# Kernel optimization log

Hardware: AMD Instinct MI355X
Metric: run time of the kernel (lower is better)

Reference implementation:

```python
import jax, jax.numpy as jnp
import numpy as np

N_NODES = 100000
N_EDGES = 3200000
NFEAT, H1, H2, NCLASS = 512, 300, 200, 40


def setup_inputs() -> dict:
    key = jax.random.key(0)
    ks = jax.random.split(key, 8)
    x = jax.random.normal(ks[0], (N_NODES, NFEAT), dtype=jnp.float32)
    edge_index = jax.random.randint(ks[1], (2, N_EDGES), 0, N_NODES, dtype=jnp.int32)
    edge_weight = jax.random.uniform(ks[2], (N_EDGES,), dtype=jnp.float32)
    def glorot(k, fi, fo):
        s = 1.0 / np.sqrt(fi)
        return jax.random.uniform(k, (fi, fo), jnp.float32, -s, s)
    w1 = glorot(ks[3], NFEAT, H1)
    w2 = glorot(ks[4], H1, H2)
    w3 = glorot(ks[5], H2, NCLASS)
    return {
        'x': x, 'edge_index': edge_index, 'edge_weight': edge_weight,
        'w1': w1, 'b1': jnp.zeros((H1,), jnp.float32),
        'w2': w2, 'b2': jnp.zeros((H2,), jnp.float32),
        'w3': w3, 'b3': jnp.zeros((NCLASS,), jnp.float32),
    }


def _gcn_layer(h, edge_index, edge_weight, w, b):
    # support = h @ W ; out = A @ support + b  (A given as weighted edge list)
    support = h @ w                                   # [N, out]
    src, dst = edge_index[0], edge_index[1]
    msgs = support[src] * edge_weight[:, None]        # gather + scale, [E, out]
    agg = jax.ops.segment_sum(msgs, dst, num_segments=h.shape[0])
    return agg + b


def reference(x, edge_index, edge_weight, w1, b1, w2, b2, w3, b3):
    h1 = jax.nn.relu(_gcn_layer(x, edge_index, edge_weight, w1, b1))
    h2 = jax.nn.relu(_gcn_layer(h1, edge_index, edge_weight, w2, b2))
    logits = _gcn_layer(h2, edge_index, edge_weight, w3, b3)
    return jax.nn.softmax(logits, axis=1)
```

## Files before the change

kernel.cpp:

```cpp
#include <hip/hip_runtime.h>
#include <hip/hip_bf16.h>
#include <hip/hip_fp16.h>
#include <math.h>

#define NFEAT 512
#define H1 300
#define H2 200
#define NCLASS 40

typedef __attribute__((ext_vector_type(8))) _Float16 half8;
typedef __attribute__((ext_vector_type(4))) float f32x4;
typedef __attribute__((ext_vector_type(2))) unsigned int u32x2;

__device__ __forceinline__ void stage16(const void* gptr, void* ldsptr) {
    __builtin_amdgcn_global_load_lds(
        (const __attribute__((address_space(1))) unsigned int*)gptr,
        (__attribute__((address_space(3))) unsigned int*)ldsptr,
        16, 0, 0);
}

__device__ __forceinline__ unsigned short f2h(float f) {
    return __half_as_ushort(__float2half(f));
}
__device__ __forceinline__ float h2f(unsigned short u) {
    return __half2float(__ushort_as_half(u));
}
__device__ __forceinline__ float2 h2f2(unsigned int u) {
    __half2 h = *reinterpret_cast<__half2*>(&u);
    return __half22float2(h);
}
__device__ __forceinline__ unsigned pack2h(float a, float b) {
    return (unsigned)f2h(a) | ((unsigned)f2h(b) << 16);
}


__global__ __launch_bounds__(256) void count_dst_kernel(const int* __restrict__ dst,
                                                        int* __restrict__ counts, int E) {
    int i = blockIdx.x * blockDim.x + threadIdx.x;
    if (i < E) atomicAdd(&counts[dst[i]], 1);
}

__global__ __launch_bounds__(1024) void scan_kernel(const int* __restrict__ counts,
                                                    int* __restrict__ row_ptr,
                                                    int* __restrict__ nextp, int N) {
    __shared__ int sums[1024];
    const int tid = threadIdx.x;
    const int CH = (N + 1023) >> 10;
    const int b = tid * CH;
    const int e = min(b + CH, N);
    int s = 0;
    for (int i = b; i < e; i++) s += counts[i];
    sums[tid] = s;
    __syncthreads();
    #pragma unroll
    for (int off = 1; off < 1024; off <<= 1) {
        int t = (tid >= off) ? sums[tid - off] : 0;
        __syncthreads();
        sums[tid] += t;
        __syncthreads();
    }
    int run = (tid > 0) ? sums[tid - 1] : 0;
    for (int i = b; i < e; i++) {
        row_ptr[i] = run;
        nextp[i] = run;
        run += counts[i];
    }
    if (tid == 0) row_ptr[N] = sums[1023];
}


__global__ __launch_bounds__(256) void fill_csr_pass_kernel(const int* __restrict__ src,
                                                            const int* __restrict__ dst,
                                                            const float* __restrict__ ew,
                                                            int* __restrict__ next,
                                                            int2* __restrict__ csr_sw,
                                                            int E, int lo, int hi) {
    int i = blockIdx.x * blockDim.x + threadIdx.x;
    if (i < E) {
        int d = dst[i];
        if (d >= lo && d < hi) {
            int pos = atomicAdd(&next[d], 1);
            csr_sw[pos] = make_int2(src[i], __float_as_int(ew[i]));
        }
    }
}


__global__ __launch_bounds__(256) void split_weights_kernel(
        const float* __restrict__ w1, const float* __restrict__ w2, const float* __restrict__ w3,
        unsigned short* __restrict__ W1H, unsigned short* __restrict__ W1L,
        unsigned short* __restrict__ W2H, unsigned short* __restrict__ W2L,
        unsigned short* __restrict__ W3H, unsigned short* __restrict__ W3L) {
    int i = blockIdx.x * 256 + threadIdx.x;
    const float* w; unsigned short *H, *L; int K, N, KP;
    if (i < 163840) {
        w = w1; H = W1H; L = W1L; K = 512; N = 300; KP = 512;
    } else if (i < 163840 + 81920) {
        i -= 163840; w = w2; H = W2H; L = W2L; K = 300; N = 200; KP = 320;
    } else {
        i -= 245760; w = w3; H = W3H; L = W3L; K = 200; N = 40; KP = 256;
    }
    int n = i / KP, k = i - n * KP;
    float a = (n < N && k < K) ? w[(size_t)k * N + n] : 0.f;
    unsigned short h = f2h(a);
    H[i] = h;
    L[i] = f2h(a - h2f(h));
}


template <int KPAD, int NT, bool AF32>
__global__ __launch_bounds__(256, 3) void gemm_f16_kernel(
        const void* __restrict__ A_,
        const unsigned short* __restrict__ Bhi, const unsigned short* __restrict__ Blo,
        unsigned short* __restrict__ C, int M, int NP, int MT) {
    __shared__ short Bs_hi[4096];
    __shared__ short Bs_lo[4096];

    const int id = blockIdx.x;
    const int g  = id / (8 * NT);
    const int r  = id % (8 * NT);
    const int nt = r >> 3;
    const int x  = r & 7;
    const int mt = g * 8 + x;
    if (mt >= MT) return;

    const int tid = threadIdx.x;
    const int wave = tid >> 6, lane = tid & 63;
    const int lm = lane & 15, quad = lane >> 4;
    const int bm = mt * 256, bn = nt * 64;

    f32x4 acc[4][4] = {};

    for (int k0 = 0; k0 < KPAD; k0 += 64) {
        #pragma unroll
        for (int i = 0; i < 2; i++) {
            int t = i * 256 + tid;
            int n = t >> 3;
            int c = (t & 7) ^ (n & 7);
            size_t goff = (size_t)(bn + n) * KPAD + (size_t)(k0 + c * 8);
            int lbase = (i * 256 + wave * 64) * 8;
            stage16(Bhi + goff, Bs_hi + lbase);
            stage16(Blo + goff, Bs_lo + lbase);
        }
        __syncthreads();

        #pragma unroll
        for (int h = 0; h < 2; h++) {
            const int cidx = h * 4 + quad;
            half8 a[4], bh[4], bl[4];
            #pragma unroll
            for (int i = 0; i < 4; i++) {
                int row = bm + wave * 64 + i * 16 + lm;
                row = row < M ? row : M - 1;
                size_t off = (size_t)row * KPAD + (size_t)(k0 + cidx * 8);
                if (AF32) {
                    const float* ap = (const float*)A_ + off;
                    float4 p = *(const float4*)ap;
                    float4 q = *(const float4*)(ap + 4);
                    half8 t8;
                    t8[0] = (_Float16)p.x; t8[1] = (_Float16)p.y;
                    t8[2] = (_Float16)p.z; t8[3] = (_Float16)p.w;
                    t8[4] = (_Float16)q.x; t8[5] = (_Float16)q.y;
                    t8[6] = (_Float16)q.z; t8[7] = (_Float16)q.w;
                    a[i] = t8;
                } else {
                    a[i] = *(const half8*)((const unsigned short*)A_ + off);
                }
            }
            #pragma unroll
            for (int j = 0; j < 4; j++) {
                int n = j * 16 + lm;
                int off = (n * 8 + (cidx ^ (n & 7))) * 8;
                bh[j] = *(const half8*)(Bs_hi + off);
                bl[j] = *(const half8*)(Bs_lo + off);
            }
            #pragma unroll
            for (int i = 0; i < 4; i++)
                #pragma unroll
                for (int j = 0; j < 4; j++) {
                    acc[i][j] = __builtin_amdgcn_mfma_f32_16x16x32_f16(a[i], bh[j], acc[i][j], 0, 0, 0);
                    acc[i][j] = __builtin_amdgcn_mfma_f32_16x16x32_f16(a[i], bl[j], acc[i][j], 0, 0, 0);
                }
        }
        __syncthreads();
    }

    #pragma unroll
    for (int i = 0; i < 4; i++) {
        #pragma unroll
        for (int j = 0; j < 4; j++) {
            #pragma unroll
            for (int r2 = 0; r2 < 4; r2++) {
                int row = bm + wave * 64 + i * 16 + quad * 4 + r2;
                int col = bn + j * 16 + lm;
                if (row < M && col < NP)
                    C[(size_t)row * NP + col] = f2h(acc[i][j][r2]);
            }
        }
    }
}


template <int F, int NPS, int NPO>
__global__ __launch_bounds__(256) void spmm_relu_f16_kernel(
        const int* __restrict__ row_ptr, const int2* __restrict__ csr_sw,
        const unsigned short* __restrict__ support, const float* __restrict__ bias,
        unsigned short* __restrict__ outp, int N) {
    constexpr int F4 = F / 4;
    constexpr int NP4 = NPO / 4;
    constexpr int NCH = (F4 + 63) / 64;
    constexpr int NCHW = (NP4 + 63) / 64;

    int row = blockIdx.x * 4 + (threadIdx.x >> 6);
    int lane = threadIdx.x & 63;
    if (row >= N) return;
    int beg = row_ptr[row], end = row_ptr[row + 1];

    float acc[NCHW][4] = {};

    int e = beg;
    int nb8 = (end - beg) >> 3;
    if (nb8 > 0) {
        int2 swbuf[8];
        #pragma unroll
        for (int q = 0; q < 8; q++) swbuf[q] = csr_sw[e + q];
        for (int b = 0; b < nb8; b++) {
            int s_[8]; float w_[8];
            #pragma unroll
            for (int q = 0; q < 8; q++) {
                s_[q] = __builtin_amdgcn_readfirstlane(swbuf[q].x);
                w_[q] = __uint_as_float((unsigned)__builtin_amdgcn_readfirstlane(swbuf[q].y));
            }
            u32x2 u[8][NCH];
            #pragma unroll
            for (int q = 0; q < 8; q++) {
                const unsigned short* sp = support + (size_t)s_[q] * NPS;
                #pragma unroll
                for (int j = 0; j < NCH; j++) {
                    int f4 = j * 64 + lane;
                    if (f4 < F4) u[q][j] = *(const u32x2*)(sp + f4 * 4);
                }
            }
            int enext = e + 8;
            if (b + 1 < nb8) {
                #pragma unroll
                for (int q = 0; q < 8; q++) swbuf[q] = csr_sw[enext + q];
            }
            #pragma unroll
            for (int q = 0; q < 8; q++) {
                #pragma unroll
                for (int j = 0; j < NCH; j++) {
                    int f4 = j * 64 + lane;
                    if (f4 < F4) {
                        float2 a0 = h2f2(u[q][j].x), a1 = h2f2(u[q][j].y);
                        acc[j][0] += w_[q] * a0.x;
                        acc[j][1] += w_[q] * a0.y;
                        acc[j][2] += w_[q] * a1.x;
                        acc[j][3] += w_[q] * a1.y;
                    }
                }
            }
            e = enext;
        }
    }
    for (; e + 3 < end; e += 4) {
        int s_[4]; float w_[4];
        #pragma unroll
        for (int q = 0; q < 4; q++) {
            int2 sw = csr_sw[e + q];
            s_[q] = __builtin_amdgcn_readfirstlane(sw.x);
            w_[q] = __uint_as_float((unsigned)__builtin_amdgcn_readfirstlane(sw.y));
        }
        u32x2 u[4][NCH];
        #pragma unroll
        for (int q = 0; q < 4; q++) {
            const unsigned short* sp = support + (size_t)s_[q] * NPS;
            #pragma unroll
            for (int j = 0; j < NCH; j++) {
                int f4 = j * 64 + lane;
                if (f4 < F4) u[q][j] = *(const u32x2*)(sp + f4 * 4);
            }
        }
        #pragma unroll
        for (int q = 0; q < 4; q++) {
            #pragma unroll
            for (int j = 0; j < NCH; j++) {
                int f4 = j * 64 + lane;
                if (f4 < F4) {
                    float2 a0 = h2f2(u[q][j].x), a1 = h2f2(u[q][j].y);
                    acc[j][0] += w_[q] * a0.x;
                    acc[j][1] += w_[q] * a0.y;
                    acc[j][2] += w_[q] * a1.x;
                    acc[j][3] += w_[q] * a1.y;
                }
            }
        }
    }
    for (; e < end; e++) {
        int2 sw = csr_sw[e];
        int ssrc = __builtin_amdgcn_readfirstlane(sw.x);
        float w0 = __uint_as_float((unsigned)__builtin_amdgcn_readfirstlane(sw.y));
        const unsigned short* sp = support + (size_t)ssrc * NPS;
        #pragma unroll
        for (int j = 0; j < NCH; j++) {
            int f4 = j * 64 + lane;
            if (f4 < F4) {
                u32x2 u = *(const u32x2*)(sp + f4 * 4);
                float2 a0 = h2f2(u.x), a1 = h2f2(u.y);
                acc[j][0] += w0 * a0.x;
                acc[j][1] += w0 * a0.y;
                acc[j][2] += w0 * a1.x;
                acc[j][3] += w0 * a1.y;
            }
        }
    }

    #pragma unroll
    for (int j = 0; j < NCHW; j++) {
        int f4 = j * 64 + lane;
        if (f4 < NP4) {
            bool real = f4 < F4;
            float4 bb = real ? ((const float4*)bias)[f4] : make_float4(0, 0, 0, 0);
            float v0 = real ? fmaxf(acc[j][0] + bb.x, 0.f) : 0.f;
            float v1 = real ? fmaxf(acc[j][1] + bb.y, 0.f) : 0.f;
            float v2 = real ? fmaxf(acc[j][2] + bb.z, 0.f) : 0.f;
            float v3 = real ? fmaxf(acc[j][3] + bb.w, 0.f) : 0.f;
            u32x2 w;
            w.x = pack2h(v0, v1);
            w.y = pack2h(v2, v3);
            *(u32x2*)(outp + (size_t)row * NPO + f4 * 4) = w;
        }
    }
}


__global__ __launch_bounds__(256) void spmm_softmax_kernel(
        const int* __restrict__ row_ptr, const int2* __restrict__ csr_sw,
        const unsigned short* __restrict__ support, const float* __restrict__ bias,
        float* __restrict__ out, int N) {
    int row = blockIdx.x * 4 + (threadIdx.x >> 6);
    int lane = threadIdx.x & 63;
    if (row >= N) return;
    int beg = row_ptr[row], end = row_ptr[row + 1];

    const int g = lane / 20;
    const int t = lane - g * 20;
    const bool lact = lane < 60;

    float a0 = 0.f, a1 = 0.f;
    for (int e = beg; e < end; e += 3) {
        int ei = e + g;
        bool v = lact && (ei < end);
        int2 sw = csr_sw[v ? ei : beg];
        float w = v ? __int_as_float(sw.y) : 0.f;
        unsigned u = *(const unsigned*)(support + (size_t)sw.x * 40 + t * 2);
        float2 aa = h2f2(u);
        a0 += w * aa.x;
        a1 += w * aa.y;
    }
    a0 += __shfl(a0, lane + 20) + __shfl(a0, lane + 40);
    a1 += __shfl(a1, lane + 20) + __shfl(a1, lane + 40);

    const bool act = lane < 20;
    float v0 = 0.f, v1 = 0.f, m = -INFINITY;
    if (act) {
        float2 bb = ((const float2*)bias)[t];
        v0 = a0 + bb.x;
        v1 = a1 + bb.y;
        m = fmaxf(v0, v1);
    }
    #pragma unroll
    for (int off = 16; off; off >>= 1) m = fmaxf(m, __shfl_xor(m, off));
    float e0 = 0.f, e1 = 0.f;
    if (act) { e0 = expf(v0 - m); e1 = expf(v1 - m); }
    float s = e0 + e1;
    #pragma unroll
    for (int off = 16; off; off >>= 1) s += __shfl_xor(s, off);
    if (act) {
        float inv = 1.f / s;
        *(float2*)(out + (size_t)row * NCLASS + t * 2) = make_float2(e0 * inv, e1 * inv);
    }
}


extern "C" void kernel_launch(void* const* d_in, const int* in_sizes, int n_in,
                              void* d_out, int out_size, void* d_ws, size_t ws_size,
                              hipStream_t stream) {
    const float* x   = (const float*)d_in[0];
    const int*   ei  = (const int*)d_in[1];
    const float* ew  = (const float*)d_in[2];
    const float* w1  = (const float*)d_in[3];
    const float* b1  = (const float*)d_in[4];
    const float* w2  = (const float*)d_in[5];
    const float* b2  = (const float*)d_in[6];
    const float* w3  = (const float*)d_in[7];
    const float* b3  = (const float*)d_in[8];
    float* out = (float*)d_out;

    const int N = in_sizes[0] / NFEAT;
    const int E = in_sizes[2];
    const int* src = ei;
    const int* dst = ei + E;

    const int KP1 = 512, NP1 = 320, NT1 = 5;
    const int KP2 = 320, NP2 = 200, NT2 = 4;
    const int KP3 = 256, NP3 = 40,  NT3 = 1;

    char* base = (char*)d_ws;
    unsigned short* H1H = (unsigned short*)(base);
    unsigned short* H2H = (unsigned short*)(base);

    unsigned short* support = (unsigned short*)(base + 102400256);

    size_t wo = 102400256 + 64000256;
    auto walloc = [&](size_t bytes) { void* r = base + wo; wo += (bytes + 255) & ~(size_t)255; return r; };
    unsigned short* W1H = (unsigned short*)walloc((size_t)320 * 512 * 2);
    unsigned short* W1L = (unsigned short*)walloc((size_t)320 * 512 * 2);
    unsigned short* W2H = (unsigned short*)walloc((size_t)256 * 320 * 2);
    unsigned short* W2L = (unsigned short*)walloc((size_t)256 * 320 * 2);
    unsigned short* W3H = (unsigned short*)walloc((size_t)64 * 256 * 2);
    unsigned short* W3L = (unsigned short*)walloc((size_t)64 * 256 * 2);
    int*  counts  = (int*)walloc((size_t)N * 4);
    int*  row_ptr = (int*)walloc((size_t)(N + 1) * 4);
    int*  nextp   = (int*)walloc((size_t)N * 4);
    int2* csr_sw  = (int2*)walloc((size_t)E * 8);

    const int MT = (N + 255) / 256;
    const int G  = (MT + 7) / 8;
    const int wgs = (N + 3) / 4;
    const int EB = (E + 255) / 256;

    hipMemsetAsync(counts, 0, (size_t)N * 4, stream);
    count_dst_kernel<<<EB, 256, 0, stream>>>(dst, counts, E);
    scan_kernel<<<1, 1024, 0, stream>>>(counts, row_ptr, nextp, N);
    {
        const int P = 8;
        const int CHN = (N + P - 1) / P;
        for (int p = 0; p < P; p++) {
            int lo = p * CHN;
            int hi = min(N, lo + CHN);
            fill_csr_pass_kernel<<<EB, 256, 0, stream>>>(src, dst, ew, nextp, csr_sw, E, lo, hi);
        }
    }

    split_weights_kernel<<<1024, 256, 0, stream>>>(w1, w2, w3, W1H, W1L, W2H, W2L, W3H, W3L);

    gemm_f16_kernel<KP1, NT1, true><<<G * 8 * NT1, 256, 0, stream>>>(
        x, W1H, W1L, support, N, NP1, MT);
    spmm_relu_f16_kernel<H1, 320, 320><<<wgs, 256, 0, stream>>>(row_ptr, csr_sw, support, b1, H1H, N);

    gemm_f16_kernel<KP2, NT2, false><<<G * 8 * NT2, 256, 0, stream>>>(
        H1H, W2H, W2L, support, N, NP2, MT);
    spmm_relu_f16_kernel<H2, 200, 256><<<wgs, 256, 0, stream>>>(row_ptr, csr_sw, support, b2, H2H, N);

    gemm_f16_kernel<KP3, NT3, false><<<G * 8 * NT3, 256, 0, stream>>>(
        H2H, W3H, W3L, support, N, NP3, MT);
    spmm_softmax_kernel<<<wgs, 256, 0, stream>>>(row_ptr, csr_sw, support, b3, out, N);
}
```

Before: 1.625 ms.

## Parallelize CSR prefix scan across blocks and widen SpMM gathers to 16 bytes

Replaces the single-block 1024-thread scan with a three-kernel multi-block scan (block sums, block offsets, fill), so the row-pointer build uses many CUs instead of one. Also restructures the ReLU SpMM so each lane loads 8 halfs with one 16-byte load instead of several 8-byte chunks, which cuts load instruction count. Lanes beyond F/8 sit idle, and two extra kernel launches are added.

```diff
diff --git a/kernel.cpp b/kernel.cpp
--- a/kernel.cpp
+++ b/kernel.cpp
@@ -40,32 +40,71 @@
     if (i < E) atomicAdd(&counts[dst[i]], 1);
 }
 
-__global__ __launch_bounds__(1024) void scan_kernel(const int* __restrict__ counts,
-                                                    int* __restrict__ row_ptr,
-                                                    int* __restrict__ nextp, int N) {
-    __shared__ int sums[1024];
-    const int tid = threadIdx.x;
-    const int CH = (N + 1023) >> 10;
-    const int b = tid * CH;
-    const int e = min(b + CH, N);
+#define SCAN_NB 256
+
+__global__ __launch_bounds__(256) void scan_blocksum_kernel(const int* __restrict__ counts,
+                                                            int* __restrict__ bsum, int N) {
+    __shared__ int red[256];
+    const int b = blockIdx.x, t = threadIdx.x;
+    const int CHB = (N + SCAN_NB - 1) / SCAN_NB;
+    const int lo = b * CHB, hi = min(lo + CHB, N);
     int s = 0;
-    for (int i = b; i < e; i++) s += counts[i];
-    sums[tid] = s;
+    for (int i = lo + t; i < hi; i += 256) s += counts[i];
+    red[t] = s;
     __syncthreads();
     #pragma unroll
-    for (int off = 1; off < 1024; off <<= 1) {
-        int t = (tid >= off) ? sums[tid - off] : 0;
-        __syncthreads();
-        sums[tid] += t;
-        __syncthreads();
-    }
-    int run = (tid > 0) ? sums[tid - 1] : 0;
-    for (int i = b; i < e; i++) {
+    for (int off = 128; off; off >>= 1) {
+        if (t < off) red[t] += red[t + off];
+        __syncthreads();
+    }
+    if (t == 0) bsum[b] = red[0];
+}
+
+__global__ __launch_bounds__(256) void scan_boff_kernel(const int* __restrict__ bsum,
+                                                        int* __restrict__ boff,
+                                                        int* __restrict__ row_ptr, int N) {
+    __shared__ int s[256];
+    const int t = threadIdx.x;
+    s[t] = bsum[t];
+    __syncthreads();
+    #pragma unroll
+    for (int off = 1; off < 256; off <<= 1) {
+        int v = (t >= off) ? s[t - off] : 0;
+        __syncthreads();
+        s[t] += v;
+        __syncthreads();
+    }
+    boff[t] = (t > 0) ? s[t - 1] : 0;
+    if (t == 255) row_ptr[N] = s[255];
+}
+
+__global__ __launch_bounds__(256) void scan_fill_kernel(const int* __restrict__ counts,
+                                                        const int* __restrict__ boff,
+                                                        int* __restrict__ row_ptr,
+                                                        int* __restrict__ nextp, int N) {
+    __shared__ int red[256];
+    const int b = blockIdx.x, t = threadIdx.x;
+    const int CHB = (N + SCAN_NB - 1) / SCAN_NB;
+    const int lo = b * CHB, hi = min(lo + CHB, N);
+    const int CHT = (CHB + 255) / 256;
+    const int tl = min(lo + t * CHT, hi), th = min(tl + CHT, hi);
+    int s = 0;
+    for (int i = tl; i < th; i++) s += counts[i];
+    red[t] = s;
+    __syncthreads();
+    #pragma unroll
+    for (int off = 1; off < 256; off <<= 1) {
+        int v = (t >= off) ? red[t - off] : 0;
+        __syncthreads();
+        red[t] += v;
+        __syncthreads();
+    }
+    int run = boff[b] + ((t > 0) ? red[t - 1] : 0);
+    for (int i = tl; i < th; i++) {
         row_ptr[i] = run;
         nextp[i] = run;
         run += counts[i];
     }
-    if (tid == 0) row_ptr[N] = sums[1023];
 }
 
 
@@ -206,17 +245,15 @@
         const int* __restrict__ row_ptr, const int2* __restrict__ csr_sw,
         const unsigned short* __restrict__ support, const float* __restrict__ bias,
         unsigned short* __restrict__ outp, int N) {
-    constexpr int F4 = F / 4;
-    constexpr int NP4 = NPO / 4;
-    constexpr int NCH = (F4 + 63) / 64;
-    constexpr int NCHW = (NP4 + 63) / 64;
+    constexpr int LPE = (F + 7) / 8;
 
     int row = blockIdx.x * 4 + (threadIdx.x >> 6);
     int lane = threadIdx.x & 63;
     if (row >= N) return;
     int beg = row_ptr[row], end = row_ptr[row + 1];
-
-    float acc[NCHW][4] = {};
+    const bool lact = lane < LPE;
+
+    float acc[8] = {};
 
     int e = beg;
     int nb8 = (end - beg) >> 3;
@@ -231,15 +268,11 @@
                 s_[q] = __builtin_amdgcn_readfirstlane(swbuf[q].x);
                 w_[q] = __uint_as_float((unsigned)__builtin_amdgcn_readfirstlane(swbuf[q].y));
             }
-            u32x2 u[8][NCH];
-            #pragma unroll
-            for (int q = 0; q < 8; q++) {
-                const unsigned short* sp = support + (size_t)s_[q] * NPS;
+            uint4 u[8];
+            if (lact) {
                 #pragma unroll
-                for (int j = 0; j < NCH; j++) {
-                    int f4 = j * 64 + lane;
-                    if (f4 < F4) u[q][j] = *(const u32x2*)(sp + f4 * 4);
-                }
+                for (int q = 0; q < 8; q++)
+                    u[q] = *(const uint4*)(support + (size_t)s_[q] * NPS + lane * 8);
             }
             int enext = e + 8;
             if (b + 1 < nb8) {
@@ -248,17 +281,11 @@
             }
             #pragma unroll
             for (int q = 0; q < 8; q++) {
-                #pragma unroll
-                for (int j = 0; j < NCH; j++) {
-                    int f4 = j * 64 + lane;
-                    if (f4 < F4) {
-                        float2 a0 = h2f2(u[q][j].x), a1 = h2f2(u[q][j].y);
-                        acc[j][0] += w_[q] * a0.x;
-                        acc[j][1] += w_[q] * a0.y;
-                        acc[j][2] += w_[q] * a1.x;
-                        acc[j][3] += w_[q] * a1.y;
-                    }
-                }
+                float2 a;
+                a = h2f2(u[q].x); acc[0] += w_[q] * a.x; acc[1] += w_[q] * a.y;
+                a = h2f2(u[q].y); acc[2] += w_[q] * a.x; acc[3] += w_[q] * a.y;
+                a = h2f2(u[q].z); acc[4] += w_[q] * a.x; acc[5] += w_[q] * a.y;
+                a = h2f2(u[q].w); acc[6] += w_[q] * a.x; acc[7] += w_[q] * a.y;
             }
             e = enext;
         }
@@ -271,65 +298,45 @@
             s_[q] = __builtin_amdgcn_readfirstlane(sw.x);
             w_[q] = __uint_as_float((unsigned)__builtin_amdgcn_readfirstlane(sw.y));
         }
-        u32x2 u[4][NCH];
+        uint4 u[4];
+        if (lact) {
+            #pragma unroll
+            for (int q = 0; q < 4; q++)
+                u[q] = *(const uint4*)(support + (size_t)s_[q] * NPS + lane * 8);
+        }
         #pragma unroll
         for (int q = 0; q < 4; q++) {
-            const unsigned short* sp = support + (size_t)s_[q] * NPS;
-            #pragma unroll
-            for (int j = 0; j < NCH; j++) {
-                int f4 = j * 64 + lane;
-                if (f4 < F4) u[q][j] = *(const u32x2*)(sp + f4 * 4);
-            }
-        }
-        #pragma unroll
-        for (int q = 0; q < 4; q++) {
-            #pragma unroll
-            for (int j = 0; j < NCH; j++) {
-                int f4 = j * 64 + lane;
-                if (f4 < F4) {
-                    float2 a0 = h2f2(u[q][j].x), a1 = h2f2(u[q][j].y);
-                    acc[j][0] += w_[q] * a0.x;
-                    acc[j][1] += w_[q] * a0.y;
-                    acc[j][2] += w_[q] * a1.x;
-                    acc[j][3] += w_[q] * a1.y;
-                }
-            }
+            float2 a;
+            a = h2f2(u[q].x); acc[0] += w_[q] * a.x; acc[1] += w_[q] * a.y;
+            a = h2f2(u[q].y); acc[2] += w_[q] * a.x; acc[3] += w_[q] * a.y;
+            a = h2f2(u[q].z); acc[4] += w_[q] * a.x; acc[5] += w_[q] * a.y;
+            a = h2f2(u[q].w); acc[6] += w_[q] * a.x; acc[7] += w_[q] * a.y;
         }
     }
     for (; e < end; e++) {
         int2 sw = csr_sw[e];
         int ssrc = __builtin_amdgcn_readfirstlane(sw.x);
         float w0 = __uint_as_float((unsigned)__builtin_amdgcn_readfirstlane(sw.y));
-        const unsigned short* sp = support + (size_t)ssrc * NPS;
-        #pragma unroll
-        for (int j = 0; j < NCH; j++) {
-            int f4 = j * 64 + lane;
-            if (f4 < F4) {
-                u32x2 u = *(const u32x2*)(sp + f4 * 4);
-                float2 a0 = h2f2(u.x), a1 = h2f2(u.y);
-                acc[j][0] += w0 * a0.x;
-                acc[j][1] += w0 * a0.y;
-                acc[j][2] += w0 * a1.x;
-                acc[j][3] += w0 * a1.y;
-            }
-        }
-    }
-
-    #pragma unroll
-    for (int j = 0; j < NCHW; j++) {
-        int f4 = j * 64 + lane;
-        if (f4 < NP4) {
-            bool real = f4 < F4;
-            float4 bb = real ? ((const float4*)bias)[f4] : make_float4(0, 0, 0, 0);
-            float v0 = real ? fmaxf(acc[j][0] + bb.x, 0.f) : 0.f;
-            float v1 = real ? fmaxf(acc[j][1] + bb.y, 0.f) : 0.f;
-            float v2 = real ? fmaxf(acc[j][2] + bb.z, 0.f) : 0.f;
-            float v3 = real ? fmaxf(acc[j][3] + bb.w, 0.f) : 0.f;
-            u32x2 w;
-            w.x = pack2h(v0, v1);
-            w.y = pack2h(v2, v3);
-            *(u32x2*)(outp + (size_t)row * NPO + f4 * 4) = w;
-        }
+        if (lact) {
+            uint4 u = *(const uint4*)(support + (size_t)ssrc * NPS + lane * 8);
+            float2 a;
+            a = h2f2(u.x); acc[0] += w0 * a.x; acc[1] += w0 * a.y;
+            a = h2f2(u.y); acc[2] += w0 * a.x; acc[3] += w0 * a.y;
+            a = h2f2(u.z); acc[4] += w0 * a.x; acc[5] += w0 * a.y;
+            a = h2f2(u.w); acc[6] += w0 * a.x; acc[7] += w0 * a.y;
+        }
+    }
+
+    if (lane * 8 < NPO) {
+        half8 o;
+        #pragma unroll
+        for (int k = 0; k < 8; k++) {
+            int f = lane * 8 + k;
+            float v = 0.f;
+            if (f < F) v = fmaxf(acc[k] + bias[f], 0.f);
+            o[k] = (_Float16)v;
+        }
+        *(half8*)(outp + (size_t)row * NPO + lane * 8) = o;
     }
 }
 
@@ -423,6 +430,8 @@
     int*  counts  = (int*)walloc((size_t)N * 4);
     int*  row_ptr = (int*)walloc((size_t)(N + 1) * 4);
     int*  nextp   = (int*)walloc((size_t)N * 4);
+    int*  bsum    = (int*)walloc(256 * 4);
+    int*  boff    = (int*)walloc(256 * 4);
     int2* csr_sw  = (int2*)walloc((size_t)E * 8);
 
     const int MT = (N + 255) / 256;
@@ -432,7 +441,9 @@
 
     hipMemsetAsync(counts, 0, (size_t)N * 4, stream);
     count_dst_kernel<<<EB, 256, 0, stream>>>(dst, counts, E);
-    scan_kernel<<<1, 1024, 0, stream>>>(counts, row_ptr, nextp, N);
+    scan_blocksum_kernel<<<SCAN_NB, 256, 0, stream>>>(counts, bsum, N);
+    scan_boff_kernel<<<1, 256, 0, stream>>>(bsum, boff, row_ptr, N);
+    scan_fill_kernel<<<SCAN_NB, 256, 0, stream>>>(counts, boff, row_ptr, nextp, N);
     {
         const int P = 8;
         const int CHN = (N + P - 1) / P;
```

New measurement: 1.429 ms. 1.14x faster.
